# Kernel tuning notes

Measured on AMD Instinct MI355X. Metric: run time of the kernel, lower is better.

Reference implementation:

```python
import jax, jax.numpy as jnp
import numpy as np

TOP_K = 2
EPS = 1e-20


def setup_inputs() -> dict:
    key = jax.random.key(0)
    ks = jax.random.split(key, 8)
    B, S, H, E, D = 4, 2048, 1024, 8, 2048
    s = 0.02
    return {
        "x":  jax.random.normal(ks[0], (B, S, H), dtype=jnp.float32),
        "Wr": jax.random.normal(ks[1], (H, E), dtype=jnp.float32) * s,
        "Wg": jax.random.normal(ks[2], (E, H, D), dtype=jnp.float32) * s,
        "Wu": jax.random.normal(ks[3], (E, H, D), dtype=jnp.float32) * s,
        "Wd": jax.random.normal(ks[4], (E, D, H), dtype=jnp.float32) * s,
        "Sg": jax.random.normal(ks[5], (H, D), dtype=jnp.float32) * s,
        "Su": jax.random.normal(ks[6], (H, D), dtype=jnp.float32) * s,
        "Sd": jax.random.normal(ks[7], (D, H), dtype=jnp.float32) * s,
    }


def reference(x, Wr, Wg, Wu, Wd, Sg, Su, Sd):
    B, S, H = x.shape
    T = B * S
    xt = x.reshape(T, H)

    # Router: softmax scores, top-k, renormalize top-k weights
    scores = jax.nn.softmax(xt @ Wr, axis=-1)            # [T, E]
    topk_w, topk_idx = jax.lax.top_k(scores, TOP_K)      # [T, K]
    topk_w = topk_w / (topk_w.sum(axis=-1, keepdims=True) + EPS)

    # Per-expert SwiGLU FFN computed densely over all tokens (vectorized over E)
    g = jax.nn.silu(jnp.einsum('th,ehd->etd', xt, Wg))   # [E, T, D]
    u = jnp.einsum('th,ehd->etd', xt, Wu)                # [E, T, D]
    out_all = jnp.einsum('etd,edh->eth', g * u, Wd)      # [E, T, H]

    # Combine: gather each token's top-k expert outputs, weighted sum
    tok = jnp.arange(T)[:, None]                          # [T, 1]
    gathered = out_all[topk_idx, tok, :]                  # [T, K, H]
    out = jnp.sum(gathered * topk_w[..., None], axis=1).reshape(B, S, H)

    # Shared expert (applied to original input, added to MoE output)
    shared = (jax.nn.silu(x @ Sg) * (x @ Su)) @ Sd        # [B, S, H]
    return out + shared
```

## Files before the change

kernel.cpp:

```cpp
#include <hip/hip_runtime.h>
#include <stdint.h>

#define T_TOK 8192
#define HD 1024
#define ED 8
#define DD 2048
#define BM 128
#define BK 32
#define TILE_SHARED 64
#define TILE_MAX 200
#define ROWCAP 25600
#define RT_TPW 8

typedef short short8 __attribute__((ext_vector_type(8)));
typedef float f32x4 __attribute__((ext_vector_type(4)));

__device__ __forceinline__ unsigned short f2bf(float f) {
  union { float f; unsigned int u; } v; v.f = f;
  unsigned int r = (v.u + 0x7fffu + ((v.u >> 16) & 1u)) >> 16;
  return (unsigned short)r;
}

__device__ __forceinline__ void gll16(const void* g, void* l) {
  __builtin_amdgcn_global_load_lds(
      (const __attribute__((address_space(1))) unsigned int*)g,
      (__attribute__((address_space(3))) unsigned int*)l, 16, 0, 0);
}

__global__ __launch_bounds__(256) void k_zero(float* __restrict__ outp) {
  size_t i = (size_t)blockIdx.x * 256 + threadIdx.x;
  ((float4*)outp)[i] = make_float4(0.f, 0.f, 0.f, 0.f);
}

__global__ __launch_bounds__(256) void k_init(int* counts, int* tok, float* wrow) {
  int i = blockIdx.x * 256 + threadIdx.x;
  if (i < 32) counts[i] = 0;
  if (i < ROWCAP) {
    tok[i] = (i < T_TOK) ? i : 0;
    wrow[i] = (i < T_TOK) ? 1.0f : 0.0f;
  }
}

__global__ __launch_bounds__(256) void k_transpose(const float* __restrict__ in,
    unsigned short* __restrict__ outp, int R, int C) {
  __shared__ float tile[32][33];
  size_t boff = (size_t)blockIdx.z * (size_t)R * (size_t)C;
  in += boff; outp += boff;
  int c0 = blockIdx.x * 32, r0 = blockIdx.y * 32;
  int tx = threadIdx.x & 31, ty = threadIdx.x >> 5;
#pragma unroll
  for (int i = 0; i < 4; ++i)
    tile[ty + i * 8][tx] = in[(size_t)(r0 + ty + i * 8) * C + c0 + tx];
  __syncthreads();
#pragma unroll
  for (int i = 0; i < 4; ++i)
    outp[(size_t)(c0 + ty + i * 8) * R + r0 + tx] = f2bf(tile[tx][ty + i * 8]);
}

__global__ __launch_bounds__(256) void k_router(const float* __restrict__ x,
    const float* __restrict__ Wr, unsigned short* __restrict__ xb,
    int* __restrict__ counts, int* __restrict__ topE, float* __restrict__ topW) {
  __shared__ float wrT[ED * HD];
  __shared__ int hist[ED];
  int tid = threadIdx.x;
  if (tid < ED) hist[tid] = 0;
  for (int i = tid; i < ED * HD; i += 256) {
    int e = i >> 10, h = i & (HD - 1);
    wrT[i] = Wr[h * ED + e];
  }
  __syncthreads();
  int lane = tid & 63, wave = tid >> 6;
  int tbase = (blockIdx.x * 4 + wave) * RT_TPW;
  for (int tt = 0; tt < RT_TPW; ++tt) {
    int t = tbase + tt;
    const float* xrow = x + (size_t)t * HD;
    unsigned short* xbrow = xb + (size_t)t * HD;
    float acc[ED] = {0, 0, 0, 0, 0, 0, 0, 0};
#pragma unroll
    for (int i = 0; i < HD / 64; ++i) {
      int h = i * 64 + lane;
      float v = xrow[h];
      xbrow[h] = f2bf(v);
#pragma unroll
      for (int e = 0; e < ED; ++e) acc[e] += v * wrT[e * HD + h];
    }
#pragma unroll
    for (int off = 32; off; off >>= 1)
#pragma unroll
      for (int e = 0; e < ED; ++e) acc[e] += __shfl_xor(acc[e], off);
    if (lane == 0) {
      float m = acc[0];
#pragma unroll
      for (int e = 1; e < ED; ++e) m = fmaxf(m, acc[e]);
      float p[ED], s = 0.f;
#pragma unroll
      for (int e = 0; e < ED; ++e) { p[e] = __expf(acc[e] - m); s += p[e]; }
      int i0 = 0;
#pragma unroll
      for (int e = 1; e < ED; ++e) if (acc[e] > acc[i0]) i0 = e;
      int i1 = -1;
#pragma unroll
      for (int e = 0; e < ED; ++e) {
        if (e == i0) continue;
        if (i1 < 0 || acc[e] > acc[i1]) i1 = e;
      }
      float p0 = p[i0] / s, p1 = p[i1] / s;
      float rs = p0 + p1 + 1e-20f;
      topE[t * 2] = i0; topE[t * 2 + 1] = i1;
      topW[t * 2] = p0 / rs; topW[t * 2 + 1] = p1 / rs;
      atomicAdd(&hist[i0], 1);
      atomicAdd(&hist[i1], 1);
    }
  }
  __syncthreads();
  if (tid < ED) atomicAdd(&counts[tid], hist[tid]);
}

__global__ __launch_bounds__(256) void k_plan(const int* __restrict__ counts, int* cursor,
    int* __restrict__ tileE, int* __restrict__ tileEnd) {
  __shared__ int tstart[ED + 1], segend[ED];
  if (threadIdx.x == 0) {
    int base = T_TOK, rt = TILE_SHARED;
    for (int e = 0; e < ED; ++e) {
      int c = counts[e];
      cursor[e] = base;
      tstart[e] = rt;
      segend[e] = base + c;
      int tiles = (c + BM - 1) >> 7;
      rt += tiles;
      base += tiles << 7;
    }
    tstart[ED] = rt;
  }
  __syncthreads();
  for (int rt = threadIdx.x; rt < TILE_MAX; rt += 256) {
    int e = -1, end = 0;
    if (rt < TILE_SHARED) { e = ED; end = T_TOK; }
    else {
      for (int q = 0; q < ED; ++q)
        if (rt >= tstart[q] && rt < tstart[q + 1]) { e = q; end = segend[q]; }
    }
    tileE[rt] = e; tileEnd[rt] = end;
  }
}

__global__ __launch_bounds__(256) void k_scatter(const int* __restrict__ topE,
    const float* __restrict__ topW, int* cursor, int* tok, float* wrow) {
  __shared__ int lcount[ED], lbase[ED];
  int tid = threadIdx.x;
  if (tid < ED) lcount[tid] = 0;
  __syncthreads();
  int t = blockIdx.x * 256 + tid;
  int e0 = topE[t * 2], e1 = topE[t * 2 + 1];
  float w0 = topW[t * 2], w1 = topW[t * 2 + 1];
  int s0 = atomicAdd(&lcount[e0], 1);
  int s1 = atomicAdd(&lcount[e1], 1);
  __syncthreads();
  if (tid < ED) lbase[tid] = atomicAdd(&cursor[tid], lcount[tid]);
  __syncthreads();
  int p0 = lbase[e0] + s0;
  int p1 = lbase[e1] + s1;
  tok[p0] = t; wrow[p0] = w0;
  tok[p1] = t; wrow[p1] = w1;
}


__global__ __launch_bounds__(256, 2) void k_gemm1(
    const unsigned short* __restrict__ xb,
    const unsigned short* __restrict__ wgt, const unsigned short* __restrict__ wut,
    const unsigned short* __restrict__ sgt, const unsigned short* __restrict__ sut,
    const int* __restrict__ tok, const int* __restrict__ tileE,
    const int* __restrict__ tileEnd, unsigned short* __restrict__ hbuf, int tileBase) {
  int lt = blockIdx.y;
  int rt = tileBase + lt;
  int e = tileE[rt];
  if (e < 0) return;
  int n0 = blockIdx.x * BM;
  int grow0 = rt * BM;
  int hrow0 = lt * BM;
  int segEnd = tileEnd[rt];
  const unsigned short* bg = (e == ED) ? sgt : wgt + (size_t)e * DD * HD;
  const unsigned short* bu = (e == ED) ? sut : wut + (size_t)e * DD * HD;

  __shared__ __align__(16) unsigned short As[BM * BK];
  __shared__ __align__(16) unsigned short Bg[BM * BK];
  __shared__ __align__(16) unsigned short Bu[BM * BK];

  int tid = threadIdx.x, lane = tid & 63, wave = tid >> 6;
  int wm = (wave & 1) * 64, wn = (wave >> 1) * 64;
  int kc = (lane & 3) ^ ((lane >> 3) & 3);

  int ldsU[2];
  const unsigned short *pA[2], *pBg[2], *pBu[2];
#pragma unroll
  for (int r = 0; r < 2; ++r) {
    int chunk = r * 4 + wave;
    int row = chunk * 16 + (lane >> 2);
    ldsU[r] = chunk * 512;
    pA[r]  = xb + (size_t)tok[grow0 + row] * HD + kc * 8;
    pBg[r] = bg + (size_t)(n0 + row) * HD + kc * 8;
    pBu[r] = bu + (size_t)(n0 + row) * HD + kc * 8;
  }

  f32x4 zero = {0.f, 0.f, 0.f, 0.f};
  f32x4 accg[4][4], accu[4][4];
#pragma unroll
  for (int i = 0; i < 4; ++i)
#pragma unroll
    for (int j = 0; j < 4; ++j) { accg[i][j] = zero; accu[i][j] = zero; }

  int m15 = lane & 15;
  int sl8 = (((lane >> 4) ^ ((lane >> 1) & 3)) * 8);

  for (int k0 = 0; k0 < HD; k0 += BK) {
#pragma unroll
    for (int r = 0; r < 2; ++r) {
      gll16(pA[r] + k0,  As + ldsU[r]);
      gll16(pBg[r] + k0, Bg + ldsU[r]);
      gll16(pBu[r] + k0, Bu + ldsU[r]);
    }
    __syncthreads();
    short8 af[4], bgf[4], buf_[4];
#pragma unroll
    for (int i = 0; i < 4; ++i) {
      af[i]   = *(const short8*)(As + (wm + i * 16 + m15) * BK + sl8);
      bgf[i]  = *(const short8*)(Bg + (wn + i * 16 + m15) * BK + sl8);
      buf_[i] = *(const short8*)(Bu + (wn + i * 16 + m15) * BK + sl8);
    }
#pragma unroll
    for (int i = 0; i < 4; ++i)
#pragma unroll
      for (int j = 0; j < 4; ++j) {
        accg[i][j] = __builtin_amdgcn_mfma_f32_16x16x32_bf16(af[i], bgf[j],  accg[i][j], 0, 0, 0);
        accu[i][j] = __builtin_amdgcn_mfma_f32_16x16x32_bf16(af[i], buf_[j], accu[i][j], 0, 0, 0);
      }
    __syncthreads();
  }

  int colB = n0 + wn + m15;
  int rowB = wm + ((lane >> 4) << 2);
#pragma unroll
  for (int i = 0; i < 4; ++i)
#pragma unroll
    for (int j = 0; j < 4; ++j)
#pragma unroll
      for (int r = 0; r < 4; ++r) {
        int lr = rowB + i * 16 + r;
        float g = accg[i][j][r], u = accu[i][j][r];
        float h = (grow0 + lr < segEnd) ? (g / (1.0f + __expf(-g))) * u : 0.0f;
        hbuf[(size_t)(hrow0 + lr) * DD + colB + j * 16] = f2bf(h);
      }
}

__global__ __launch_bounds__(256, 2) void k_gemm2(
    const unsigned short* __restrict__ hbuf,
    const unsigned short* __restrict__ wdt, const unsigned short* __restrict__ sdt,
    const int* __restrict__ tok, const int* __restrict__ tileE,
    const int* __restrict__ tileEnd, const float* __restrict__ wrow,
    float* __restrict__ outp, int tileBase) {
  int lt = blockIdx.y;
  int rt = tileBase + lt;
  int e = tileE[rt];
  if (e < 0) return;
  int n0 = blockIdx.x * BM;
  int grow0 = rt * BM;
  int hrow0 = lt * BM;
  int segEnd = tileEnd[rt];
  const unsigned short* bd = (e == ED) ? sdt : wdt + (size_t)e * HD * DD;

  __shared__ __align__(16) unsigned short As[BM * BK];
  __shared__ __align__(16) unsigned short Bs[BM * BK];

  int tid = threadIdx.x, lane = tid & 63, wave = tid >> 6;
  int wm = (wave & 1) * 64, wn = (wave >> 1) * 64;
  int kc = (lane & 3) ^ ((lane >> 3) & 3);

  int ldsU[2];
  const unsigned short *pA[2], *pB[2];
#pragma unroll
  for (int r = 0; r < 2; ++r) {
    int chunk = r * 4 + wave;
    int row = chunk * 16 + (lane >> 2);
    ldsU[r] = chunk * 512;
    pA[r] = hbuf + (size_t)(hrow0 + row) * DD + kc * 8;
    pB[r] = bd + (size_t)(n0 + row) * DD + kc * 8;
  }

  f32x4 zero = {0.f, 0.f, 0.f, 0.f};
  f32x4 acc[4][4];
#pragma unroll
  for (int i = 0; i < 4; ++i)
#pragma unroll
    for (int j = 0; j < 4; ++j) acc[i][j] = zero;

  int m15 = lane & 15;
  int sl8 = (((lane >> 4) ^ ((lane >> 1) & 3)) * 8);

  for (int k0 = 0; k0 < DD; k0 += BK) {
#pragma unroll
    for (int r = 0; r < 2; ++r) {
      gll16(pA[r] + k0, As + ldsU[r]);
      gll16(pB[r] + k0, Bs + ldsU[r]);
    }
    __syncthreads();
    short8 af[4], bf[4];
#pragma unroll
    for (int i = 0; i < 4; ++i) {
      af[i] = *(const short8*)(As + (wm + i * 16 + m15) * BK + sl8);
      bf[i] = *(const short8*)(Bs + (wn + i * 16 + m15) * BK + sl8);
    }
#pragma unroll
    for (int i = 0; i < 4; ++i)
#pragma unroll
      for (int j = 0; j < 4; ++j)
        acc[i][j] = __builtin_amdgcn_mfma_f32_16x16x32_bf16(af[i], bf[j], acc[i][j], 0, 0, 0);
    __syncthreads();
  }

  int colB = n0 + wn + m15;
  int rowB = wm + ((lane >> 4) << 2);
#pragma unroll
  for (int i = 0; i < 4; ++i)
#pragma unroll
    for (int r = 0; r < 4; ++r) {
      int grr = grow0 + rowB + i * 16 + r;
      if (grr < segEnd) {
        float w = wrow[grr];
        size_t ob = (size_t)tok[grr] * HD;
#pragma unroll
        for (int j = 0; j < 4; ++j)
          atomicAdd(&outp[ob + colB + j * 16], acc[i][j][r] * w);
      }
    }
}

extern "C" void kernel_launch(void* const* d_in, const int* in_sizes, int n_in,
                              void* d_out, int out_size, void* d_ws, size_t ws_size,
                              hipStream_t stream) {
  const float* x  = (const float*)d_in[0];
  const float* Wr = (const float*)d_in[1];
  const float* Wg = (const float*)d_in[2];
  const float* Wu = (const float*)d_in[3];
  const float* Wd = (const float*)d_in[4];
  const float* Sg = (const float*)d_in[5];
  const float* Su = (const float*)d_in[6];
  const float* Sd = (const float*)d_in[7];
  float* outp = (float*)d_out;

  size_t fixed = 0;
  auto pad = [](size_t b) { return (b + 255) & ~(size_t)255; };
  fixed += pad((size_t)T_TOK * HD * 2);
  fixed += pad((size_t)ED * DD * HD * 2) * 3;
  fixed += pad((size_t)DD * HD * 2) * 3;
  fixed += pad((size_t)ROWCAP * 4) * 2;
  fixed += pad((size_t)T_TOK * 2 * 4) * 2;
  fixed += pad(128) * 2 + pad(1024) * 2;
  int CH = TILE_MAX;
  if (fixed + pad((size_t)CH * BM * DD * 2) > ws_size) CH = TILE_MAX / 2;
  if (fixed + pad((size_t)CH * BM * DD * 2) > ws_size) return;

  char* ws = (char*)d_ws;
  size_t off = 0;
  auto alloc = [&](size_t bytes) -> char* {
    char* p = ws + off;
    off += (bytes + 255) & ~(size_t)255;
    return p;
  };
  unsigned short* xb  = (unsigned short*)alloc((size_t)T_TOK * HD * 2);
  unsigned short* wgt = (unsigned short*)alloc((size_t)ED * DD * HD * 2);
  unsigned short* wut = (unsigned short*)alloc((size_t)ED * DD * HD * 2);
  unsigned short* wdt = (unsigned short*)alloc((size_t)ED * HD * DD * 2);
  unsigned short* sgt = (unsigned short*)alloc((size_t)DD * HD * 2);
  unsigned short* sut = (unsigned short*)alloc((size_t)DD * HD * 2);
  unsigned short* sdt = (unsigned short*)alloc((size_t)HD * DD * 2);
  int* tok       = (int*)alloc((size_t)ROWCAP * 4);
  float* wrow    = (float*)alloc((size_t)ROWCAP * 4);
  int* topE      = (int*)alloc((size_t)T_TOK * 2 * 4);
  float* topW    = (float*)alloc((size_t)T_TOK * 2 * 4);
  int* counts    = (int*)alloc(128);
  int* cursor    = (int*)alloc(128);
  int* tileE     = (int*)alloc(1024);
  int* tileEnd   = (int*)alloc(1024);
  unsigned short* hbuf = (unsigned short*)alloc((size_t)CH * BM * DD * 2);

  k_zero<<<(out_size / 4 + 255) / 256, 256, 0, stream>>>(outp);
  k_init<<<(ROWCAP + 255) / 256, 256, 0, stream>>>(counts, tok, wrow);
  k_transpose<<<dim3(DD / 32, HD / 32, ED), 256, 0, stream>>>(Wg, wgt, HD, DD);
  k_transpose<<<dim3(DD / 32, HD / 32, ED), 256, 0, stream>>>(Wu, wut, HD, DD);
  k_transpose<<<dim3(HD / 32, DD / 32, ED), 256, 0, stream>>>(Wd, wdt, DD, HD);
  k_transpose<<<dim3(DD / 32, HD / 32, 1), 256, 0, stream>>>(Sg, sgt, HD, DD);
  k_transpose<<<dim3(DD / 32, HD / 32, 1), 256, 0, stream>>>(Su, sut, HD, DD);
  k_transpose<<<dim3(HD / 32, DD / 32, 1), 256, 0, stream>>>(Sd, sdt, DD, HD);
  k_router<<<T_TOK / (4 * RT_TPW), 256, 0, stream>>>(x, Wr, xb, counts, topE, topW);
  k_plan<<<1, 256, 0, stream>>>(counts, cursor, tileE, tileEnd);
  k_scatter<<<T_TOK / 256, 256, 0, stream>>>(topE, topW, cursor, tok, wrow);
  for (int cb = 0; cb < TILE_MAX; cb += CH) {
    k_gemm1<<<dim3(DD / BM, CH), 256, 0, stream>>>(xb, wgt, wut, sgt, sut, tok,
                                                   tileE, tileEnd, hbuf, cb);
    k_gemm2<<<dim3(HD / BM, CH), 256, 0, stream>>>(hbuf, wdt, sdt, tok, tileE,
                                                   tileEnd, wrow, outp, cb);
  }
}
```

Measured before the change: 765.6 us.

## Double-buffer LDS tiles in both expert GEMMs to overlap loads with MFMA

Both grouped GEMM kernels now hold two LDS buffers per operand. The first K-tile is loaded before the loop, and each iteration issues the async global-to-LDS loads for the next tile before running MFMAs on the current one. The goal is to hide global memory latency behind matrix math instead of stalling on a barrier right after each load. The cost is twice the LDS per block (48KB for gemm1), which could limit occupancy, plus a sched_barrier that constrains instruction scheduling.

```diff
diff --git a/kernel.cpp b/kernel.cpp
--- a/kernel.cpp
+++ b/kernel.cpp
@@ -182,9 +182,9 @@
   const unsigned short* bg = (e == ED) ? sgt : wgt + (size_t)e * DD * HD;
   const unsigned short* bu = (e == ED) ? sut : wut + (size_t)e * DD * HD;
 
-  __shared__ __align__(16) unsigned short As[BM * BK];
-  __shared__ __align__(16) unsigned short Bg[BM * BK];
-  __shared__ __align__(16) unsigned short Bu[BM * BK];
+  __shared__ __align__(16) unsigned short As[2][BM * BK];
+  __shared__ __align__(16) unsigned short Bg[2][BM * BK];
+  __shared__ __align__(16) unsigned short Bu[2][BM * BK];
 
   int tid = threadIdx.x, lane = tid & 63, wave = tid >> 6;
   int wm = (wave & 1) * 64, wn = (wave >> 1) * 64;
@@ -212,20 +212,32 @@
   int m15 = lane & 15;
   int sl8 = (((lane >> 4) ^ ((lane >> 1) & 3)) * 8);
 
+#pragma unroll
+  for (int r = 0; r < 2; ++r) {
+    gll16(pA[r],  &As[0][ldsU[r]]);
+    gll16(pBg[r], &Bg[0][ldsU[r]]);
+    gll16(pBu[r], &Bu[0][ldsU[r]]);
+  }
+  __syncthreads();
+
   for (int k0 = 0; k0 < HD; k0 += BK) {
-#pragma unroll
-    for (int r = 0; r < 2; ++r) {
-      gll16(pA[r] + k0,  As + ldsU[r]);
-      gll16(pBg[r] + k0, Bg + ldsU[r]);
-      gll16(pBu[r] + k0, Bu + ldsU[r]);
-    }
-    __syncthreads();
+    int b = (k0 >> 5) & 1;
+    int k1 = k0 + BK;
+    if (k1 < HD) {
+#pragma unroll
+      for (int r = 0; r < 2; ++r) {
+        gll16(pA[r] + k1,  &As[b ^ 1][ldsU[r]]);
+        gll16(pBg[r] + k1, &Bg[b ^ 1][ldsU[r]]);
+        gll16(pBu[r] + k1, &Bu[b ^ 1][ldsU[r]]);
+      }
+    }
+    __builtin_amdgcn_sched_barrier(0);
     short8 af[4], bgf[4], buf_[4];
 #pragma unroll
     for (int i = 0; i < 4; ++i) {
-      af[i]   = *(const short8*)(As + (wm + i * 16 + m15) * BK + sl8);
-      bgf[i]  = *(const short8*)(Bg + (wn + i * 16 + m15) * BK + sl8);
-      buf_[i] = *(const short8*)(Bu + (wn + i * 16 + m15) * BK + sl8);
+      af[i]   = *(const short8*)(&As[b][(wm + i * 16 + m15) * BK + sl8]);
+      bgf[i]  = *(const short8*)(&Bg[b][(wn + i * 16 + m15) * BK + sl8]);
+      buf_[i] = *(const short8*)(&Bu[b][(wn + i * 16 + m15) * BK + sl8]);
     }
 #pragma unroll
     for (int i = 0; i < 4; ++i)
@@ -268,8 +280,8 @@
   int segEnd = tileEnd[rt];
   const unsigned short* bd = (e == ED) ? sdt : wdt + (size_t)e * HD * DD;
 
-  __shared__ __align__(16) unsigned short As[BM * BK];
-  __shared__ __align__(16) unsigned short Bs[BM * BK];
+  __shared__ __align__(16) unsigned short As[2][BM * BK];
+  __shared__ __align__(16) unsigned short Bs[2][BM * BK];
 
   int tid = threadIdx.x, lane = tid & 63, wave = tid >> 6;
   int wm = (wave & 1) * 64, wn = (wave >> 1) * 64;
@@ -296,18 +308,29 @@
   int m15 = lane & 15;
   int sl8 = (((lane >> 4) ^ ((lane >> 1) & 3)) * 8);
 
+#pragma unroll
+  for (int r = 0; r < 2; ++r) {
+    gll16(pA[r], &As[0][ldsU[r]]);
+    gll16(pB[r], &Bs[0][ldsU[r]]);
+  }
+  __syncthreads();
+
   for (int k0 = 0; k0 < DD; k0 += BK) {
-#pragma unroll
-    for (int r = 0; r < 2; ++r) {
-      gll16(pA[r] + k0, As + ldsU[r]);
-      gll16(pB[r] + k0, Bs + ldsU[r]);
-    }
-    __syncthreads();
+    int b = (k0 >> 5) & 1;
+    int k1 = k0 + BK;
+    if (k1 < DD) {
+#pragma unroll
+      for (int r = 0; r < 2; ++r) {
+        gll16(pA[r] + k1, &As[b ^ 1][ldsU[r]]);
+        gll16(pB[r] + k1, &Bs[b ^ 1][ldsU[r]]);
+      }
+    }
+    __builtin_amdgcn_sched_barrier(0);
     short8 af[4], bf[4];
 #pragma unroll
     for (int i = 0; i < 4; ++i) {
-      af[i] = *(const short8*)(As + (wm + i * 16 + m15) * BK + sl8);
-      bf[i] = *(const short8*)(Bs + (wn + i * 16 + m15) * BK + sl8);
+      af[i] = *(const short8*)(&As[b][(wm + i * 16 + m15) * BK + sl8]);
+      bf[i] = *(const short8*)(&Bs[b][(wn + i * 16 + m15) * BK + sl8]);
     }
 #pragma unroll
     for (int i = 0; i < 4; ++i)
```

Measured after the change: 768.1 us. No clear change (+0.3%).
